# Kernel optimization log

Measured on AMD Instinct MI355X. Metric: run time of the kernel, lower is better.

The kernel has to match this reference:

```python
import jax, jax.numpy as jnp
import numpy as np

D_MODEL = 2048
NUM_HEADS = 32
NUM_GROUPS = 8
HEAD_DIM = D_MODEL // NUM_HEADS  # 64
HEADS_PER_GROUP = NUM_HEADS // NUM_GROUPS  # 4


def setup_inputs() -> dict:
    key = jax.random.key(0)
    ks = jax.random.split(key, 5)
    B, S = 1, 2048
    x = jax.random.normal(ks[0], (B, S, D_MODEL), dtype=jnp.float32)
    scale = 1.0 / np.sqrt(D_MODEL)
    w_q = jax.random.normal(ks[1], (D_MODEL, D_MODEL), dtype=jnp.float32) * scale
    w_k = jax.random.normal(ks[2], (D_MODEL, NUM_GROUPS * HEAD_DIM), dtype=jnp.float32) * scale
    w_v = jax.random.normal(ks[3], (D_MODEL, NUM_GROUPS * HEAD_DIM), dtype=jnp.float32) * scale
    w_o = jax.random.normal(ks[4], (D_MODEL, D_MODEL), dtype=jnp.float32) * scale
    return {"x": x, "w_q": w_q, "w_k": w_k, "w_v": w_v, "w_o": w_o}


def reference(x, w_q, w_k, w_v, w_o):
    B, S, _ = x.shape
    # projections (nn.Linear, no bias)
    q = (x @ w_q).reshape(B, S, NUM_HEADS, HEAD_DIM)          # [B,S,H,d]
    k = (x @ w_k).reshape(B, S, NUM_GROUPS, HEAD_DIM)         # [B,S,G,d]
    v = (x @ w_v).reshape(B, S, NUM_GROUPS, HEAD_DIM)
    # group queries: [B,S,G,hpg,d] so each KV group serves heads_per_group query heads
    qg = q.reshape(B, S, NUM_GROUPS, HEADS_PER_GROUP, HEAD_DIM)
    scale = 1.0 / jnp.sqrt(jnp.asarray(HEAD_DIM, dtype=x.dtype))
    # scores: [B,G,hpg,S_q,S_k] without duplicating K/V
    scores = jnp.einsum("bsghd,btgd->bghst", qg, k) * scale
    attn = jax.nn.softmax(scores, axis=-1)
    out = jnp.einsum("bghst,btgd->bsghd", attn, v)            # [B,S,G,hpg,d]
    out = out.reshape(B, S, D_MODEL)
    return out @ w_o
```

## Files before the change

### kernel.cpp

```cpp
#include <hip/hip_runtime.h>

typedef unsigned short ushort_t;
typedef __attribute__((ext_vector_type(8))) short short8;
typedef __attribute__((ext_vector_type(4))) float floatx4;

__device__ __forceinline__ unsigned short f2bf(float f) {
  unsigned int u = __float_as_uint(f);
  u += 0x7fffu + ((u >> 16) & 1u);
  return (unsigned short)(u >> 16);
}

__device__ __forceinline__ unsigned int cvt_pk_bf16(float a, float b) {
  unsigned int r;
  asm("v_cvt_pk_bf16_f32 %0, %1, %2" : "=v"(r) : "v"(a), "v"(b));
  return r;
}

__device__ __forceinline__ void gl_lds16(const void* g, void* l) {
  __builtin_amdgcn_global_load_lds((const __attribute__((address_space(1))) void*)g,
                                   (__attribute__((address_space(3))) void*)l,
                                   16, 0, 0);
}


__global__ void conv_x_kernel(const float* __restrict__ src, ushort_t* __restrict__ dst, int n4) {
  int i = blockIdx.x * blockDim.x + threadIdx.x;
  if (i >= n4) return;
  float4 v = ((const float4*)src)[i];
  union { ushort_t u[4]; unsigned long long ll; } o;
  o.u[0] = f2bf(v.x); o.u[1] = f2bf(v.y); o.u[2] = f2bf(v.z); o.u[3] = f2bf(v.w);
  ((unsigned long long*)dst)[i] = o.ll;
}

__global__ void transpose_conv(const float* __restrict__ src, ushort_t* __restrict__ dst,
                               int R, int C) {
  __shared__ float tile[32][33];
  int c0 = blockIdx.x * 32, r0 = blockIdx.y * 32;
  int tx = threadIdx.x, ty = threadIdx.y;
#pragma unroll
  for (int i = ty; i < 32; i += 8)
    tile[i][tx] = src[(long)(r0 + i) * C + c0 + tx];
  __syncthreads();
#pragma unroll
  for (int i = ty; i < 32; i += 8)
    dst[(long)(c0 + i) * R + r0 + tx] = f2bf(tile[tx][i]);
}

template <int BM, int BN, int EPI>
__global__ __launch_bounds__(256, (BM == 64 ? 4 : 3)) void gemm_bt(
    const ushort_t* __restrict__ A, const ushort_t* __restrict__ B,
    float* __restrict__ C,
    ushort_t* __restrict__ qb, ushort_t* __restrict__ kb, ushort_t* __restrict__ vb,
    int M, int N, int K) {
  constexpr int MI = BM / 32;
  constexpr int NJ = BN / 32;
  __shared__ __attribute__((aligned(16))) ushort_t As[2][BM * 32];
  __shared__ __attribute__((aligned(16))) ushort_t Bs[2][BN * 32];
  const int t = threadIdx.x;
  const int w = t >> 6, lane = t & 63;
  const int m = lane & 15, quad = lane >> 4;
  const int nwg = gridDim.x * gridDim.y;
  const int bid = blockIdx.y * gridDim.x + blockIdx.x;
  const int sw = (bid & 7) * (nwg >> 3) + (bid >> 3);
  const int m0 = (sw / gridDim.x) * BM, n0 = (sw % gridDim.x) * BN;
  const int wr = w >> 1, wc = w & 1;

  floatx4 acc[MI][NJ] = {};

  auto stage = [&](int kk, int buf) {
#pragma unroll
    for (int i = 0; i < BM / 64; ++i) {
      int c = i * 256 + t;
      gl_lds16(A + (long)(m0 + (c >> 2)) * K + kk + (c & 3) * 8,
               As[buf] + (i * 256 + w * 64) * 8);
    }
#pragma unroll
    for (int i = 0; i < BN / 64; ++i) {
      int c = i * 256 + t;
      gl_lds16(B + (long)(n0 + (c >> 2)) * K + kk + (c & 3) * 8,
               Bs[buf] + (i * 256 + w * 64) * 8);
    }
  };

  stage(0, 0);
  __syncthreads();
  int cur = 0;
  for (int kk = 0; kk < K; kk += 32) {
    if (kk + 32 < K) stage(kk + 32, cur ^ 1);
    short8 af[MI], bf[NJ];
#pragma unroll
    for (int i = 0; i < MI; ++i)
      af[i] = *(const short8*)(As[cur] + (wr * (BM / 2) + i * 16 + m) * 32 + quad * 8);
#pragma unroll
    for (int j = 0; j < NJ; ++j)
      bf[j] = *(const short8*)(Bs[cur] + (wc * (BN / 2) + j * 16 + m) * 32 + quad * 8);
#pragma unroll
    for (int i = 0; i < MI; ++i)
#pragma unroll
      for (int j = 0; j < NJ; ++j)
        acc[i][j] = __builtin_amdgcn_mfma_f32_16x16x32_bf16(af[i], bf[j], acc[i][j], 0, 0, 0);
    __syncthreads();
    cur ^= 1;
  }

#pragma unroll
  for (int i = 0; i < MI; ++i)
#pragma unroll
    for (int j = 0; j < NJ; ++j)
#pragma unroll
      for (int r = 0; r < 4; ++r) {
        float v = acc[i][j][r];
        int row = m0 + wr * (BM / 2) + i * 16 + quad * 4 + r;
        int col = n0 + wc * (BN / 2) + j * 16 + m;
        if (EPI == 1) {
          C[(long)row * N + col] = v;
        } else {
          if (col < 2048) {
            qb[((((col >> 6) * 2048) + row) << 6) | (col & 63)] = f2bf(v * 0.18033688f);
          } else if (col < 2560) {
            int g = (col - 2048) >> 6;
            kb[(((g * 2048) + row) << 6) | (col & 63)] = f2bf(v);
          } else {
            int g = (col - 2560) >> 6;
            vb[(long)((g << 6) | (col & 63)) * 2048 + row] = f2bf(v);
          }
        }
      }
}

__global__ __launch_bounds__(256, 4) void flash_kernel(
    const ushort_t* __restrict__ Q, const ushort_t* __restrict__ Kb,
    const ushort_t* __restrict__ Vb, ushort_t* __restrict__ O, int S) {
  __shared__ __attribute__((aligned(16))) ushort_t Ks[2][64 * 64];
  __shared__ __attribute__((aligned(16))) ushort_t Vs[2][64 * 64];
  __shared__ __attribute__((aligned(16))) ushort_t Ps[4 * 16 * 64];
  const int t = threadIdx.x;
  const int w = t >> 6, lane = t & 63;
  const int m = lane & 15, quad = lane >> 4;
  const int nwg = gridDim.x * gridDim.y;
  const int bid = blockIdx.y * gridDim.x + blockIdx.x;
  const int sw = (bid & 7) * (nwg >> 3) + (bid >> 3);
  const int h = sw / gridDim.x, g = h >> 2;
  const int q0 = (sw % gridDim.x) * 64;
  const ushort_t* qp = Q + (long)h * S * 64;
  const ushort_t* kp = Kb + (long)g * S * 64;
  const ushort_t* vp = Vb + (long)g * 64 * S;

  auto stage = [&](int t0, int buf) {
#pragma unroll
    for (int i = 0; i < 2; ++i) {
      int c = i * 256 + t;
      int c0 = i * 256 + w * 64;
      int sl = ((c & 3) ^ ((c >> 3) & 3)) * 8;
      gl_lds16(kp + (long)(t0 + ((c >> 2) & 63)) * 64 + (c >> 8) * 32 + sl, Ks[buf] + c0 * 8);
      gl_lds16(vp + (long)((c >> 2) & 63) * S + t0 + (c >> 8) * 32 + sl, Vs[buf] + c0 * 8);
    }
  };

  stage(0, 0);

  short8 qf[2];
#pragma unroll
  for (int kq = 0; kq < 2; ++kq)
    qf[kq] = *(const short8*)(qp + (long)(q0 + w * 16 + m) * 64 + kq * 32 + quad * 8);

  short8 ones;
#pragma unroll
  for (int z = 0; z < 8; ++z) ones[z] = (short)0x3F80;

  floatx4 lacc = {};
  floatx4 oacc[4] = {};
  char* PwB = (char*)Ps + w * 2048;
  const int psw = (m & 7) << 4;
  const int kvswz = (quad ^ ((m >> 1) & 3)) * 8;

  __syncthreads();
  int cur = 0;
  for (int t0 = 0; t0 < S; t0 += 64) {
    if (t0 + 64 < S) stage(t0 + 64, cur ^ 1);

    floatx4 sacc[4] = {};
    __builtin_amdgcn_s_setprio(1);
#pragma unroll
    for (int ct = 0; ct < 4; ++ct) {
      short8 kf0 = *(const short8*)(Ks[cur] + (ct * 16 + m) * 32 + kvswz);
      short8 kf1 = *(const short8*)(Ks[cur] + 2048 + (ct * 16 + m) * 32 + kvswz);
      sacc[ct] = __builtin_amdgcn_mfma_f32_16x16x32_bf16(kf0, qf[0], sacc[ct], 0, 0, 0);
      sacc[ct] = __builtin_amdgcn_mfma_f32_16x16x32_bf16(kf1, qf[1], sacc[ct], 0, 0, 0);
    }
    __builtin_amdgcn_s_setprio(0);

#pragma unroll
    for (int ct = 0; ct < 4; ++ct) {
      float p0 = exp2f(sacc[ct][0]);
      float p1 = exp2f(sacc[ct][1]);
      float p2 = exp2f(sacc[ct][2]);
      float p3 = exp2f(sacc[ct][3]);
      uint2 pk;
      pk.x = cvt_pk_bf16(p0, p1);
      pk.y = cvt_pk_bf16(p2, p3);
      *(uint2*)(PwB + m * 128 + ((ct * 32 + quad * 8) ^ psw)) = pk;
    }

    __builtin_amdgcn_s_setprio(1);
#pragma unroll
    for (int kt = 0; kt < 2; ++kt) {
      short8 pf = *(const short8*)(PwB + m * 128 + ((kt * 64 + quad * 16) ^ psw));
      lacc = __builtin_amdgcn_mfma_f32_16x16x32_bf16(pf, ones, lacc, 0, 0, 0);
#pragma unroll
      for (int ct = 0; ct < 4; ++ct) {
        short8 vf = *(const short8*)(Vs[cur] + kt * 2048 + (ct * 16 + m) * 32 + kvswz);
        oacc[ct] = __builtin_amdgcn_mfma_f32_16x16x32_bf16(pf, vf, oacc[ct], 0, 0, 0);
      }
    }
    __builtin_amdgcn_s_setprio(0);

    __syncthreads();
    cur ^= 1;
  }

#pragma unroll
  for (int r = 0; r < 4; ++r) {
    float inv = 1.f / lacc[r];
    int srow = q0 + w * 16 + quad * 4 + r;
#pragma unroll
    for (int ct = 0; ct < 4; ++ct)
      O[(long)srow * 2048 + h * 64 + ct * 16 + m] = f2bf(oacc[ct][r] * inv);
  }
}


extern "C" void kernel_launch(void* const* d_in, const int* in_sizes, int n_in,
                              void* d_out, int out_size, void* d_ws, size_t ws_size,
                              hipStream_t stream) {
  (void)in_sizes; (void)n_in; (void)out_size; (void)ws_size;
  const float* x  = (const float*)d_in[0];
  const float* wq = (const float*)d_in[1];
  const float* wk = (const float*)d_in[2];
  const float* wv = (const float*)d_in[3];
  const float* wo = (const float*)d_in[4];
  float* out = (float*)d_out;
  char* ws = (char*)d_ws;
  const size_t MB = 1u << 20;

  ushort_t* xb    = (ushort_t*)(ws);
  ushort_t* wqkvT = (ushort_t*)(ws + 8 * MB);
  ushort_t* woT   = (ushort_t*)(ws + 20 * MB);
  ushort_t* qbuf  = (ushort_t*)(ws + 28 * MB);
  ushort_t* kbuf  = (ushort_t*)(ws + 36 * MB);
  ushort_t* vbuf  = (ushort_t*)(ws + 38 * MB);
  ushort_t* attn  = xb;

  conv_x_kernel<<<4096, 256, 0, stream>>>(x, xb, 2048 * 2048 / 4);
  dim3 tb(32, 8);
  transpose_conv<<<dim3(64, 64), tb, 0, stream>>>(wq, wqkvT, 2048, 2048);
  transpose_conv<<<dim3(16, 64), tb, 0, stream>>>(wk, wqkvT + 2048 * 2048, 2048, 512);
  transpose_conv<<<dim3(16, 64), tb, 0, stream>>>(wv, wqkvT + 2560 * 2048, 2048, 512);
  transpose_conv<<<dim3(64, 64), tb, 0, stream>>>(wo, woT, 2048, 2048);

  gemm_bt<128, 64, 0><<<dim3(48, 16), 256, 0, stream>>>(xb, wqkvT, nullptr, qbuf, kbuf, vbuf,
                                                        2048, 3072, 2048);
  flash_kernel<<<dim3(32, 32), 256, 0, stream>>>(qbuf, kbuf, vbuf, attn, 2048);
  gemm_bt<64, 64, 1><<<dim3(32, 32), 256, 0, stream>>>(attn, woT, out, nullptr, nullptr, nullptr,
                                                       2048, 2048, 2048);
}
```

Before: 249.8 us.

## Enlarge flash attention tile to 128 queries with 8 waves, two row tiles each

```diff
diff --git a/kernel.cpp b/kernel.cpp
--- a/kernel.cpp
+++ b/kernel.cpp
@@ -128,12 +128,12 @@
       }
 }
 
-__global__ __launch_bounds__(256, 4) void flash_kernel(
+__global__ __launch_bounds__(512, 4) void flash_kernel(
     const ushort_t* __restrict__ Q, const ushort_t* __restrict__ Kb,
     const ushort_t* __restrict__ Vb, ushort_t* __restrict__ O, int S) {
   __shared__ __attribute__((aligned(16))) ushort_t Ks[2][64 * 64];
   __shared__ __attribute__((aligned(16))) ushort_t Vs[2][64 * 64];
-  __shared__ __attribute__((aligned(16))) ushort_t Ps[4 * 16 * 64];
+  __shared__ __attribute__((aligned(16))) ushort_t Ps[8 * 2 * 16 * 64];
   const int t = threadIdx.x;
   const int w = t >> 6, lane = t & 63;
   const int m = lane & 15, quad = lane >> 4;
@@ -141,36 +141,33 @@
   const int bid = blockIdx.y * gridDim.x + blockIdx.x;
   const int sw = (bid & 7) * (nwg >> 3) + (bid >> 3);
   const int h = sw / gridDim.x, g = h >> 2;
-  const int q0 = (sw % gridDim.x) * 64;
+  const int q0 = (sw % gridDim.x) * 128;
   const ushort_t* qp = Q + (long)h * S * 64;
   const ushort_t* kp = Kb + (long)g * S * 64;
   const ushort_t* vp = Vb + (long)g * 64 * S;
 
   auto stage = [&](int t0, int buf) {
-#pragma unroll
-    for (int i = 0; i < 2; ++i) {
-      int c = i * 256 + t;
-      int c0 = i * 256 + w * 64;
-      int sl = ((c & 3) ^ ((c >> 3) & 3)) * 8;
-      gl_lds16(kp + (long)(t0 + ((c >> 2) & 63)) * 64 + (c >> 8) * 32 + sl, Ks[buf] + c0 * 8);
-      gl_lds16(vp + (long)((c >> 2) & 63) * S + t0 + (c >> 8) * 32 + sl, Vs[buf] + c0 * 8);
-    }
+    int sl = ((t & 3) ^ ((t >> 3) & 3)) * 8;
+    gl_lds16(kp + (long)(t0 + ((t >> 2) & 63)) * 64 + (t >> 8) * 32 + sl, Ks[buf] + w * 512);
+    gl_lds16(vp + (long)((t >> 2) & 63) * S + t0 + (t >> 8) * 32 + sl, Vs[buf] + w * 512);
   };
 
   stage(0, 0);
 
-  short8 qf[2];
-#pragma unroll
-  for (int kq = 0; kq < 2; ++kq)
-    qf[kq] = *(const short8*)(qp + (long)(q0 + w * 16 + m) * 64 + kq * 32 + quad * 8);
+  short8 qf[2][2];
+#pragma unroll
+  for (int rt = 0; rt < 2; ++rt)
+#pragma unroll
+    for (int kq = 0; kq < 2; ++kq)
+      qf[rt][kq] = *(const short8*)(qp + (long)(q0 + w * 32 + rt * 16 + m) * 64 + kq * 32 + quad * 8);
 
   short8 ones;
 #pragma unroll
   for (int z = 0; z < 8; ++z) ones[z] = (short)0x3F80;
 
-  floatx4 lacc = {};
-  floatx4 oacc[4] = {};
-  char* PwB = (char*)Ps + w * 2048;
+  floatx4 lacc[2] = {};
+  floatx4 oacc[2][4] = {};
+  char* PwB = (char*)Ps + w * 4096;
   const int psw = (m & 7) << 4;
   const int kvswz = (quad ^ ((m >> 1) & 3)) * 8;
 
@@ -179,38 +176,49 @@
   for (int t0 = 0; t0 < S; t0 += 64) {
     if (t0 + 64 < S) stage(t0 + 64, cur ^ 1);
 
-    floatx4 sacc[4] = {};
+    floatx4 sacc[2][4] = {};
     __builtin_amdgcn_s_setprio(1);
 #pragma unroll
     for (int ct = 0; ct < 4; ++ct) {
       short8 kf0 = *(const short8*)(Ks[cur] + (ct * 16 + m) * 32 + kvswz);
       short8 kf1 = *(const short8*)(Ks[cur] + 2048 + (ct * 16 + m) * 32 + kvswz);
-      sacc[ct] = __builtin_amdgcn_mfma_f32_16x16x32_bf16(kf0, qf[0], sacc[ct], 0, 0, 0);
-      sacc[ct] = __builtin_amdgcn_mfma_f32_16x16x32_bf16(kf1, qf[1], sacc[ct], 0, 0, 0);
+#pragma unroll
+      for (int rt = 0; rt < 2; ++rt) {
+        sacc[rt][ct] = __builtin_amdgcn_mfma_f32_16x16x32_bf16(kf0, qf[rt][0], sacc[rt][ct], 0, 0, 0);
+        sacc[rt][ct] = __builtin_amdgcn_mfma_f32_16x16x32_bf16(kf1, qf[rt][1], sacc[rt][ct], 0, 0, 0);
+      }
     }
     __builtin_amdgcn_s_setprio(0);
 
 #pragma unroll
-    for (int ct = 0; ct < 4; ++ct) {
-      float p0 = exp2f(sacc[ct][0]);
-      float p1 = exp2f(sacc[ct][1]);
-      float p2 = exp2f(sacc[ct][2]);
-      float p3 = exp2f(sacc[ct][3]);
-      uint2 pk;
-      pk.x = cvt_pk_bf16(p0, p1);
-      pk.y = cvt_pk_bf16(p2, p3);
-      *(uint2*)(PwB + m * 128 + ((ct * 32 + quad * 8) ^ psw)) = pk;
-    }
+    for (int rt = 0; rt < 2; ++rt)
+#pragma unroll
+      for (int ct = 0; ct < 4; ++ct) {
+        float p0 = exp2f(sacc[rt][ct][0]);
+        float p1 = exp2f(sacc[rt][ct][1]);
+        float p2 = exp2f(sacc[rt][ct][2]);
+        float p3 = exp2f(sacc[rt][ct][3]);
+        uint2 pk;
+        pk.x = cvt_pk_bf16(p0, p1);
+        pk.y = cvt_pk_bf16(p2, p3);
+        *(uint2*)(PwB + rt * 2048 + m * 128 + ((ct * 32 + quad * 8) ^ psw)) = pk;
+      }
 
     __builtin_amdgcn_s_setprio(1);
 #pragma unroll
     for (int kt = 0; kt < 2; ++kt) {
-      short8 pf = *(const short8*)(PwB + m * 128 + ((kt * 64 + quad * 16) ^ psw));
-      lacc = __builtin_amdgcn_mfma_f32_16x16x32_bf16(pf, ones, lacc, 0, 0, 0);
+      short8 pf[2];
+#pragma unroll
+      for (int rt = 0; rt < 2; ++rt) {
+        pf[rt] = *(const short8*)(PwB + rt * 2048 + m * 128 + ((kt * 64 + quad * 16) ^ psw));
+        lacc[rt] = __builtin_amdgcn_mfma_f32_16x16x32_bf16(pf[rt], ones, lacc[rt], 0, 0, 0);
+      }
 #pragma unroll
       for (int ct = 0; ct < 4; ++ct) {
         short8 vf = *(const short8*)(Vs[cur] + kt * 2048 + (ct * 16 + m) * 32 + kvswz);
-        oacc[ct] = __builtin_amdgcn_mfma_f32_16x16x32_bf16(pf, vf, oacc[ct], 0, 0, 0);
+#pragma unroll
+        for (int rt = 0; rt < 2; ++rt)
+          oacc[rt][ct] = __builtin_amdgcn_mfma_f32_16x16x32_bf16(pf[rt], vf, oacc[rt][ct], 0, 0, 0);
       }
     }
     __builtin_amdgcn_s_setprio(0);
@@ -220,13 +228,15 @@
   }
 
 #pragma unroll
-  for (int r = 0; r < 4; ++r) {
-    float inv = 1.f / lacc[r];
-    int srow = q0 + w * 16 + quad * 4 + r;
-#pragma unroll
-    for (int ct = 0; ct < 4; ++ct)
-      O[(long)srow * 2048 + h * 64 + ct * 16 + m] = f2bf(oacc[ct][r] * inv);
-  }
+  for (int rt = 0; rt < 2; ++rt)
+#pragma unroll
+    for (int r = 0; r < 4; ++r) {
+      float inv = 1.f / lacc[rt][r];
+      int srow = q0 + w * 32 + rt * 16 + quad * 4 + r;
+#pragma unroll
+      for (int ct = 0; ct < 4; ++ct)
+        O[(long)srow * 2048 + h * 64 + ct * 16 + m] = f2bf(oacc[rt][ct][r] * inv);
+    }
 }
 
 
@@ -260,7 +270,7 @@
 
   gemm_bt<128, 64, 0><<<dim3(48, 16), 256, 0, stream>>>(xb, wqkvT, nullptr, qbuf, kbuf, vbuf,
                                                         2048, 3072, 2048);
-  flash_kernel<<<dim3(32, 32), 256, 0, stream>>>(qbuf, kbuf, vbuf, attn, 2048);
+  flash_kernel<<<dim3(16, 32), 512, 0, stream>>>(qbuf, kbuf, vbuf, attn, 2048);
   gemm_bt<64, 64, 1><<<dim3(32, 32), 256, 0, stream>>>(attn, woT, out, nullptr, nullptr, nullptr,
                                                        2048, 2048, 2048);
 }
```

Result: slower. 288.4 us (+15.4%).
